# Performance work log

Measured on AMD Instinct MI355X. Metric: run time of the kernel, lower is better.

Reference implementation:

```python
import jax, jax.numpy as jnp
import numpy as np

B, S, D = 8, 4096, 768
HEADS = 12
NEIGHBORS = 2
DILATION = 1
KERNEL = 1 + 2 * NEIGHBORS  # 5
DIM_HEAD = D // HEADS


def setup_inputs() -> dict:
    key = jax.random.key(0)
    ks = jax.random.split(key, 11)
    sc = 1.0 / np.sqrt(D)
    return {
        "x": jax.random.normal(ks[0], (B, S, D), dtype=jnp.float32),
        "Wq": jax.random.normal(ks[1], (D, D), dtype=jnp.float32) * sc,
        "bq": jax.random.normal(ks[2], (D,), dtype=jnp.float32) * 0.02,
        "Wk": jax.random.normal(ks[3], (D, D), dtype=jnp.float32) * sc,
        "bk": jax.random.normal(ks[4], (D,), dtype=jnp.float32) * 0.02,
        "Wv": jax.random.normal(ks[5], (D, D), dtype=jnp.float32) * sc,
        "bv": jax.random.normal(ks[6], (D,), dtype=jnp.float32) * 0.02,
        "Wo": jax.random.normal(ks[7], (D, D), dtype=jnp.float32) * sc,
        "bo": jax.random.normal(ks[8], (D,), dtype=jnp.float32) * 0.02,
        "gamma": jnp.ones((D,), dtype=jnp.float32),
        "beta": jnp.zeros((D,), dtype=jnp.float32),
    }


def _extract_seq_patches(x, kernel_size, dilation):
    # [B, S, D] -> [B, S, kernel_size, D] of dilated local windows, zero-padded.
    seq_len = x.shape[1]
    patch_size = kernel_size + (dilation - 1) * (kernel_size - 1)
    pad_r = (patch_size - 1) // 2
    pad_l = patch_size - pad_r - 1
    xp = jnp.pad(x, ((0, 0), (pad_l, pad_r), (0, 0)))
    # small fixed loop over kernel positions (kernel_size = 5)
    return jnp.stack([xp[:, i:i + seq_len] for i in range(0, patch_size, dilation)], axis=2)


def reference(x, Wq, bq, Wk, bk, Wv, bv, Wo, bo, gamma, beta):
    patches = _extract_seq_patches(x, KERNEL, DILATION)  # [B, S, K, D]
    q = x @ Wq + bq                                       # [B, S, D]
    k = patches @ Wk + bk                                 # [B, S, K, D]
    v = patches @ Wv + bv                                 # [B, S, K, D]
    # split heads
    q = q.reshape(B, S, HEADS, DIM_HEAD)
    k = k.reshape(B, S, KERNEL, HEADS, DIM_HEAD)
    v = v.reshape(B, S, KERNEL, HEADS, DIM_HEAD)
    scale = jnp.sqrt(jnp.asarray(DIM_HEAD, dtype=q.dtype))
    scores = jnp.einsum('bshd,bskhd->bshk', q, k) / scale  # [B, S, H, K]
    p = jax.nn.softmax(scores, axis=-1)
    att = jnp.einsum('bshk,bskhd->bshd', p, v)             # [B, S, H, dh]
    att = att.reshape(B, S, D)
    att = att @ Wo + bo
    y = att + x
    # LayerNorm over last dim
    mu = jnp.mean(y, axis=-1, keepdims=True)
    var = jnp.var(y, axis=-1, keepdims=True)
    y = (y - mu) / jnp.sqrt(var + 1e-5) * gamma + beta
    return y
```

## Files before the change

kernel.cpp:

```cpp
#include <hip/hip_runtime.h>

#define B_  8
#define S_  4096
#define D_  768
#define H_  12
#define M_  (B_ * S_)
#define NQKV_ 2304
#define NTILES 12

typedef unsigned short u16;
typedef __attribute__((ext_vector_type(4))) float  f32x4;
typedef __attribute__((ext_vector_type(8))) __bf16 bf16x8;
typedef __attribute__((ext_vector_type(4))) u16    u16x4;

#define GAS __attribute__((address_space(1)))
#define LAS __attribute__((address_space(3)))

__device__ __forceinline__ u16 f2bf(float f) {
    unsigned u = __float_as_uint(f);
    u += 0x7FFF + ((u >> 16) & 1);
    return (u16)(u >> 16);
}
__device__ __forceinline__ float bf2f(u16 h) {
    return __uint_as_float(((unsigned)h) << 16);
}

__device__ __forceinline__ void gload_lds16(const void* g, void* l) {
    __builtin_amdgcn_global_load_lds((const GAS void*)g, (LAS void*)l, 16, 0, 0);
}

__device__ __forceinline__ int xcd_swz(int bid, int nwg) {
    return (bid & 7) * (nwg >> 3) + (bid >> 3);
}

__global__ __launch_bounds__(256) void castx_kernel(const float* __restrict__ x,
                                                    u16* __restrict__ xb) {
    const int i = blockIdx.x * 256 + threadIdx.x;
    const float4 v = ((const float4*)x)[i];
    u16x4 o;
    o.x = f2bf(v.x); o.y = f2bf(v.y); o.z = f2bf(v.z); o.w = f2bf(v.w);
    ((u16x4*)xb)[i] = o;
}

__global__ __launch_bounds__(256) void wtrans_kernel(const float* __restrict__ Wq,
                                                     const float* __restrict__ Wk,
                                                     const float* __restrict__ Wv,
                                                     const float* __restrict__ Wo,
                                                     u16* __restrict__ Wb) {
    const float* W = (blockIdx.z == 0) ? Wq : (blockIdx.z == 1) ? Wk
                   : (blockIdx.z == 2) ? Wv : Wo;
    u16* O = Wb + (size_t)blockIdx.z * D_ * D_;
    __shared__ float tile[32][33];
    const int tx = threadIdx.x & 31, ty = threadIdx.x >> 5;
    const int k0 = blockIdx.y * 32, n0 = blockIdx.x * 32;
#pragma unroll
    for (int j = 0; j < 4; j++)
        tile[ty + j * 8][tx] = W[(size_t)(k0 + ty + j * 8) * D_ + n0 + tx];
    __syncthreads();
#pragma unroll
    for (int j = 0; j < 4; j++)
        O[(size_t)(n0 + ty + j * 8) * D_ + k0 + tx] = f2bf(tile[tx][ty + j * 8]);
}


#define MFMA8(AF, BF)                                                        \
    __builtin_amdgcn_s_setprio(1);                                           \
    _Pragma("unroll") for (int mi = 0; mi < 4; ++mi)                         \
        _Pragma("unroll") for (int ni = 0; ni < 2; ++ni)                     \
            acc[mi][ni] = __builtin_amdgcn_mfma_f32_16x16x32_bf16(           \
                AF[mi], BF[ni], acc[mi][ni], 0, 0, 0);                       \
    __builtin_amdgcn_s_setprio(0)

#define RD(p, imm) (*(const bf16x8*)((p) + (imm)))

template <int MODE>
__global__ __launch_bounds__(512, 4) void gemm2_kernel(
    const u16* __restrict__ A, const u16* __restrict__ Wb,
    const float* __restrict__ b0, const float* __restrict__ b1,
    const float* __restrict__ b2,
    u16* __restrict__ outb, const u16* __restrict__ xres) {
    extern __shared__ char lds[];

    const int t = threadIdx.x;
    const int w = t >> 6, l = t & 63;
    const int wm = w >> 2, wn = w & 3;

    const int NTN = (MODE == 0) ? 18 : 6;
    const int work = xcd_swz(blockIdx.x, gridDim.x);
    const int mt = work / NTN, nt = work % NTN;
    const int m0 = mt * 128;
    const int col0 = nt * 128;
    const int widx = (MODE == 0) ? (nt / 6) : 3;
    const int n0w  = (MODE == 0) ? (nt % 6) * 128 : col0;

    const int sr = w * 16 + (l >> 3);
    const int sc = l & 7;
    const int schunk = sc ^ (sr & 7);
    const u16* Asrc = A + (size_t)(m0 + sr) * D_ + schunk * 8;
    const u16* Bsrc = Wb + (size_t)widx * (D_ * D_)
                         + (size_t)(n0w + sr) * D_ + schunk * 8;
    char* const dstA = lds + w * 2048;
    char* const dstB = lds + 16384 + w * 2048;

    const int ck0 = (((l >> 4) ^ (l & 7)) << 4);
    const int ck1 = ((((l >> 4) + 4) ^ (l & 7)) << 4);
    const char* aB = lds + (wm * 64 + (l & 15)) * 128;
    const char* bB = lds + 16384 + (wn * 32 + (l & 15)) * 128;

    f32x4 acc[4][2];
#pragma unroll
    for (int i = 0; i < 4; i++)
#pragma unroll
        for (int j = 0; j < 2; j++) acc[i][j] = (f32x4){0.f, 0.f, 0.f, 0.f};

    auto STAGE = [&](int tk, int b) {
        const int ko = tk * 64;
        char* da = dstA + b * 32768;
        char* db = dstB + b * 32768;
        gload_lds16(Asrc + ko, da);
        gload_lds16(Asrc + ko + 8 * D_, da + 1024);
        gload_lds16(Bsrc + ko, db);
        gload_lds16(Bsrc + ko + 8 * D_, db + 1024);
    };

    STAGE(0, 0);
    __syncthreads();

#pragma unroll
    for (int X = 0; X < NTILES; ++X) {
        const int cb = (X & 1) * 32768;
        if (X + 1 < NTILES) STAGE(X + 1, (X & 1) ^ 1);

        bf16x8 af[4], bf[2];
#pragma unroll
        for (int mi = 0; mi < 4; ++mi) af[mi] = RD(aB, cb + mi * 2048 + ck0);
#pragma unroll
        for (int ni = 0; ni < 2; ++ni) bf[ni] = RD(bB, cb + ni * 2048 + ck0);
        MFMA8(af, bf);
#pragma unroll
        for (int mi = 0; mi < 4; ++mi) af[mi] = RD(aB, cb + mi * 2048 + ck1);
#pragma unroll
        for (int ni = 0; ni < 2; ++ni) bf[ni] = RD(bB, cb + ni * 2048 + ck1);
        MFMA8(af, bf);

        __syncthreads();
    }

    const int crow0 = m0 + wm * 64 + ((l >> 4) << 2);
    const int ccol0 = col0 + wn * 32 + (l & 15);
    if (MODE == 0) {
        const float* bias = (widx == 0) ? b0 : (widx == 1) ? b1 : b2;
        const int bcol0 = ccol0 - widx * D_;
#pragma unroll
        for (int mi = 0; mi < 4; ++mi)
#pragma unroll
            for (int ni = 0; ni < 2; ++ni) {
                const float bv = bias[bcol0 + ni * 16];
#pragma unroll
                for (int r = 0; r < 4; ++r)
                    outb[(size_t)(crow0 + mi * 16 + r) * NQKV_ + ccol0 + ni * 16] =
                        f2bf(acc[mi][ni][r] + bv);
            }
    } else {
#pragma unroll
        for (int mi = 0; mi < 4; ++mi)
#pragma unroll
            for (int ni = 0; ni < 2; ++ni) {
                const int col = ccol0 + ni * 16;
                const float bv = b0[col];
#pragma unroll
                for (int r = 0; r < 4; ++r) {
                    const size_t idx = (size_t)(crow0 + mi * 16 + r) * D_ + col;
                    outb[idx] = f2bf(acc[mi][ni][r] + bv + bf2f(xres[idx]));
                }
            }
    }
}

__global__ __launch_bounds__(256) void attn_kernel(const u16* __restrict__ QKV,
                                                   const float* __restrict__ bk,
                                                   const float* __restrict__ bv,
                                                   u16* __restrict__ att) {
    const int gw = xcd_swz(blockIdx.x, gridDim.x) * 4 + (threadIdx.x >> 6);
    const int l  = threadIdx.x & 63;
    const int hq = gw % 3;
    const int m  = gw / 3;
    const int s  = m & (S_ - 1);
    const int col = hq * 256 + l * 4;
    const u16* base = QKV + (size_t)m * NQKV_;

    const u16x4 qv = *(const u16x4*)(base + col);
    float qf[4];
#pragma unroll
    for (int j = 0; j < 4; j++) qf[j] = bf2f(qv[j]);

    float sc[5];
#pragma unroll
    for (int i = 0; i < 5; i++) {
        const int sp = s + i - 2;
        float p;
        if (sp >= 0 && sp < S_) {
            const u16x4 kv = *(const u16x4*)(base + (i - 2) * NQKV_ + D_ + col);
            p = qf[0] * bf2f(kv[0]) + qf[1] * bf2f(kv[1])
              + qf[2] * bf2f(kv[2]) + qf[3] * bf2f(kv[3]);
        } else {
            const float4 kb = *(const float4*)(bk + col);
            p = qf[0] * kb.x + qf[1] * kb.y + qf[2] * kb.z + qf[3] * kb.w;
        }
#pragma unroll
        for (int off = 1; off < 16; off <<= 1) p += __shfl_xor(p, off, 64);
        sc[i] = p * 0.125f;
    }
    float mx = sc[0];
#pragma unroll
    for (int i = 1; i < 5; i++) mx = fmaxf(mx, sc[i]);
    float e[5], sum = 0.f;
#pragma unroll
    for (int i = 0; i < 5; i++) { e[i] = __expf(sc[i] - mx); sum += e[i]; }
    const float inv = 1.f / sum;

    float o[4] = {0.f, 0.f, 0.f, 0.f};
#pragma unroll
    for (int i = 0; i < 5; i++) {
        const float wgt = e[i] * inv;
        const int sp = s + i - 2;
        if (sp >= 0 && sp < S_) {
            const u16x4 vv = *(const u16x4*)(base + (i - 2) * NQKV_ + 2 * D_ + col);
#pragma unroll
            for (int j = 0; j < 4; j++) o[j] += wgt * bf2f(vv[j]);
        } else {
            const float4 vb = *(const float4*)(bv + col);
            o[0] += wgt * vb.x; o[1] += wgt * vb.y;
            o[2] += wgt * vb.z; o[3] += wgt * vb.w;
        }
    }
    u16x4 ov;
#pragma unroll
    for (int j = 0; j < 4; j++) ov[j] = f2bf(o[j]);
    *(u16x4*)(att + (size_t)m * D_ + col) = ov;
}

__global__ __launch_bounds__(256) void ln_kernel(const u16* __restrict__ Yb,
                                                 const float* __restrict__ gamma,
                                                 const float* __restrict__ beta,
                                                 float* __restrict__ out) {
    const int row = blockIdx.x;
    const u16* r = Yb + (size_t)row * D_;
    const int t = threadIdx.x;
    const float v0 = bf2f(r[t]), v1 = bf2f(r[t + 256]), v2 = bf2f(r[t + 512]);
    float s  = v0 + v1 + v2;
    float s2 = v0 * v0 + v1 * v1 + v2 * v2;
#pragma unroll
    for (int off = 32; off > 0; off >>= 1) {
        s  += __shfl_xor(s,  off, 64);
        s2 += __shfl_xor(s2, off, 64);
    }
    __shared__ float red[8];
    const int w = t >> 6, l = t & 63;
    if (l == 0) { red[w] = s; red[4 + w] = s2; }
    __syncthreads();
    s  = red[0] + red[1] + red[2] + red[3];
    s2 = red[4] + red[5] + red[6] + red[7];
    const float mu  = s * (1.f / 768.f);
    const float var = s2 * (1.f / 768.f) - mu * mu;
    const float inv = rsqrtf(var + 1e-5f);
    float* o = out + (size_t)row * D_;
    o[t]       = (v0 - mu) * inv * gamma[t]       + beta[t];
    o[t + 256] = (v1 - mu) * inv * gamma[t + 256] + beta[t + 256];
    o[t + 512] = (v2 - mu) * inv * gamma[t + 512] + beta[t + 512];
}

extern "C" void kernel_launch(void* const* d_in, const int* in_sizes, int n_in,
                              void* d_out, int out_size, void* d_ws, size_t ws_size,
                              hipStream_t stream) {
    const float* x     = (const float*)d_in[0];
    const float* Wq    = (const float*)d_in[1];
    const float* bq    = (const float*)d_in[2];
    const float* Wk    = (const float*)d_in[3];
    const float* bk    = (const float*)d_in[4];
    const float* Wv    = (const float*)d_in[5];
    const float* bv    = (const float*)d_in[6];
    const float* Wo    = (const float*)d_in[7];
    const float* bo    = (const float*)d_in[8];
    const float* gamma = (const float*)d_in[9];
    const float* beta  = (const float*)d_in[10];

    char* ws = (char*)d_ws;
    u16*   Wb  = (u16*)ws;
    u16*   xb  = (u16*)(ws + 4718592);
    u16*   QKV = (u16*)(ws + 4718592 + 50331648);
    u16*   yb  = QKV;
    u16*   att = (u16*)d_out;

    (void)hipFuncSetAttribute(reinterpret_cast<const void*>(&gemm2_kernel<0>),
                              hipFuncAttributeMaxDynamicSharedMemorySize, 65536);
    (void)hipFuncSetAttribute(reinterpret_cast<const void*>(&gemm2_kernel<1>),
                              hipFuncAttributeMaxDynamicSharedMemorySize, 65536);

    castx_kernel<<<(M_ * D_) / (256 * 4), 256, 0, stream>>>(x, xb);
    wtrans_kernel<<<dim3(24, 24, 4), 256, 0, stream>>>(Wq, Wk, Wv, Wo, Wb);
    gemm2_kernel<0><<<(M_ / 128) * 18, 512, 65536, stream>>>(xb, Wb, bq, bk, bv,
                                                             QKV, nullptr);
    attn_kernel<<<(M_ * 3) / 4, 256, 0, stream>>>(QKV, bk, bv, att);
    gemm2_kernel<1><<<(M_ / 128) * 6, 512, 65536, stream>>>(att, Wb, bo, nullptr, nullptr,
                                                            yb, xb);
    ln_kernel<<<M_, 256, 0, stream>>>(yb, gamma, beta, (float*)d_out);
}
```

Baseline: 294.4 us.

## Make GEMM kernels persistent with cross-tile prefetch of next tile's first K-slice

Both projection GEMMs now launch 512 persistent blocks, each handling a contiguous run of output tiles (9 for QKV, 3 for output projection). The first K-slice of the next tile is staged into LDS while the last slice of the current tile is computed, and the epilogue runs inside the final K iteration. The aim is to hide per-tile prologue latency and reduce block launch overhead. In exchange, occupancy drops to one wave of blocks, tail balance is fixed, and the xcd swizzle now maps to contiguous work ranges, which may change L2 reuse.

```diff
diff --git a/kernel.cpp b/kernel.cpp
--- a/kernel.cpp
+++ b/kernel.cpp
@@ -74,7 +74,7 @@
 #define RD(p, imm) (*(const bf16x8*)((p) + (imm)))
 
 template <int MODE>
-__global__ __launch_bounds__(512, 4) void gemm2_kernel(
+__global__ __launch_bounds__(512, 4) void gemmp_kernel(
     const u16* __restrict__ A, const u16* __restrict__ Wb,
     const float* __restrict__ b0, const float* __restrict__ b1,
     const float* __restrict__ b2,
@@ -86,94 +86,115 @@
     const int wm = w >> 2, wn = w & 3;
 
     const int NTN = (MODE == 0) ? 18 : 6;
-    const int work = xcd_swz(blockIdx.x, gridDim.x);
-    const int mt = work / NTN, nt = work % NTN;
-    const int m0 = mt * 128;
-    const int col0 = nt * 128;
-    const int widx = (MODE == 0) ? (nt / 6) : 3;
-    const int n0w  = (MODE == 0) ? (nt % 6) * 128 : col0;
-
-    const int sr = w * 16 + (l >> 3);
-    const int sc = l & 7;
-    const int schunk = sc ^ (sr & 7);
-    const u16* Asrc = A + (size_t)(m0 + sr) * D_ + schunk * 8;
-    const u16* Bsrc = Wb + (size_t)widx * (D_ * D_)
-                         + (size_t)(n0w + sr) * D_ + schunk * 8;
-    char* const dstA = lds + w * 2048;
-    char* const dstB = lds + 16384 + w * 2048;
+    const int NW  = (MODE == 0) ? 9 : 3;
+    int work = xcd_swz(blockIdx.x, gridDim.x) * NW;
+
+    const int lrow = l >> 3;
+    const int schunk = (l & 7) ^ lrow;
 
     const int ck0 = (((l >> 4) ^ (l & 7)) << 4);
     const int ck1 = ((((l >> 4) + 4) ^ (l & 7)) << 4);
     const char* aB = lds + (wm * 64 + (l & 15)) * 128;
     const char* bB = lds + 16384 + (wn * 32 + (l & 15)) * 128;
 
+    int m0, col0, widx;
+    const u16 *As, *Bs;
+    auto setp = [&](int wk, int& _m0, int& _col0, int& _widx,
+                    const u16*& _As, const u16*& _Bs) {
+        const int mt = wk / NTN, nt = wk % NTN;
+        _m0 = mt * 128;
+        _col0 = nt * 128;
+        _widx = (MODE == 0) ? (nt / 6) : 3;
+        const int n0w = (MODE == 0) ? (nt % 6) * 128 : _col0;
+        _As = A + (size_t)(_m0 + w * 16 + lrow) * D_ + schunk * 8;
+        _Bs = Wb + (size_t)_widx * (D_ * D_)
+                 + (size_t)(n0w + w * 16 + lrow) * D_ + schunk * 8;
+    };
+    setp(work, m0, col0, widx, As, Bs);
+
+    auto STAGE = [&](const u16* _A, const u16* _B, int kt, int bo) {
+        const int ko = kt * 64;
+        char* da = lds + bo + w * 2048;
+        char* db = lds + bo + 16384 + w * 2048;
+        gload_lds16(_A + ko, da);
+        gload_lds16(_A + ko + 8 * D_, da + 1024);
+        gload_lds16(_B + ko, db);
+        gload_lds16(_B + ko + 8 * D_, db + 1024);
+    };
+
     f32x4 acc[4][2];
 #pragma unroll
     for (int i = 0; i < 4; i++)
 #pragma unroll
         for (int j = 0; j < 2; j++) acc[i][j] = (f32x4){0.f, 0.f, 0.f, 0.f};
 
-    auto STAGE = [&](int tk, int b) {
-        const int ko = tk * 64;
-        char* da = dstA + b * 32768;
-        char* db = dstB + b * 32768;
-        gload_lds16(Asrc + ko, da);
-        gload_lds16(Asrc + ko + 8 * D_, da + 1024);
-        gload_lds16(Bsrc + ko, db);
-        gload_lds16(Bsrc + ko + 8 * D_, db + 1024);
-    };
-
-    STAGE(0, 0);
+    STAGE(As, Bs, 0, 0);
     __syncthreads();
 
-#pragma unroll
-    for (int X = 0; X < NTILES; ++X) {
-        const int cb = (X & 1) * 32768;
-        if (X + 1 < NTILES) STAGE(X + 1, (X & 1) ^ 1);
-
-        bf16x8 af[4], bf[2];
-#pragma unroll
-        for (int mi = 0; mi < 4; ++mi) af[mi] = RD(aB, cb + mi * 2048 + ck0);
-#pragma unroll
-        for (int ni = 0; ni < 2; ++ni) bf[ni] = RD(bB, cb + ni * 2048 + ck0);
-        MFMA8(af, bf);
-#pragma unroll
-        for (int mi = 0; mi < 4; ++mi) af[mi] = RD(aB, cb + mi * 2048 + ck1);
-#pragma unroll
-        for (int ni = 0; ni < 2; ++ni) bf[ni] = RD(bB, cb + ni * 2048 + ck1);
-        MFMA8(af, bf);
-
-        __syncthreads();
-    }
-
-    const int crow0 = m0 + wm * 64 + ((l >> 4) << 2);
-    const int ccol0 = col0 + wn * 32 + (l & 15);
-    if (MODE == 0) {
-        const float* bias = (widx == 0) ? b0 : (widx == 1) ? b1 : b2;
-        const int bcol0 = ccol0 - widx * D_;
-#pragma unroll
-        for (int mi = 0; mi < 4; ++mi)
-#pragma unroll
-            for (int ni = 0; ni < 2; ++ni) {
-                const float bv = bias[bcol0 + ni * 16];
-#pragma unroll
-                for (int r = 0; r < 4; ++r)
-                    outb[(size_t)(crow0 + mi * 16 + r) * NQKV_ + ccol0 + ni * 16] =
-                        f2bf(acc[mi][ni][r] + bv);
+    for (int j = 0; j < NW; ++j) {
+        int nm0 = m0, ncol0 = col0, nwidx = widx;
+        const u16 *nAs = As, *nBs = Bs;
+        if (j + 1 < NW) setp(work + 1, nm0, ncol0, nwidx, nAs, nBs);
+
+#pragma unroll
+        for (int kt = 0; kt < 12; ++kt) {
+            const int cb = (kt & 1) * 32768;
+            const int ob = cb ^ 32768;
+            if (kt < 11)          STAGE(As, Bs, kt + 1, ob);
+            else if (j + 1 < NW)  STAGE(nAs, nBs, 0, ob);
+
+            bf16x8 af[4], bf[2];
+#pragma unroll
+            for (int mi = 0; mi < 4; ++mi) af[mi] = RD(aB, cb + mi * 2048 + ck0);
+#pragma unroll
+            for (int ni = 0; ni < 2; ++ni) bf[ni] = RD(bB, cb + ni * 2048 + ck0);
+            MFMA8(af, bf);
+#pragma unroll
+            for (int mi = 0; mi < 4; ++mi) af[mi] = RD(aB, cb + mi * 2048 + ck1);
+#pragma unroll
+            for (int ni = 0; ni < 2; ++ni) bf[ni] = RD(bB, cb + ni * 2048 + ck1);
+            MFMA8(af, bf);
+
+            if (kt == 11) {
+                const int crow0 = m0 + wm * 64 + ((l >> 4) << 2);
+                const int ccol0 = col0 + wn * 32 + (l & 15);
+                if (MODE == 0) {
+                    const float* bias = (widx == 0) ? b0 : (widx == 1) ? b1 : b2;
+                    const int bcol0 = ccol0 - widx * D_;
+#pragma unroll
+                    for (int mi = 0; mi < 4; ++mi)
+#pragma unroll
+                        for (int ni = 0; ni < 2; ++ni) {
+                            const float bv = bias[bcol0 + ni * 16];
+#pragma unroll
+                            for (int r = 0; r < 4; ++r)
+                                outb[(size_t)(crow0 + mi * 16 + r) * NQKV_
+                                     + ccol0 + ni * 16] = f2bf(acc[mi][ni][r] + bv);
+                        }
+                } else {
+#pragma unroll
+                    for (int mi = 0; mi < 4; ++mi)
+#pragma unroll
+                        for (int ni = 0; ni < 2; ++ni) {
+                            const int col = ccol0 + ni * 16;
+                            const float bv = b0[col];
+#pragma unroll
+                            for (int r = 0; r < 4; ++r) {
+                                const size_t idx =
+                                    (size_t)(crow0 + mi * 16 + r) * D_ + col;
+                                outb[idx] = f2bf(acc[mi][ni][r] + bv + bf2f(xres[idx]));
+                            }
+                        }
+                }
+#pragma unroll
+                for (int i = 0; i < 4; i++)
+#pragma unroll
+                    for (int jj = 0; jj < 2; jj++)
+                        acc[i][jj] = (f32x4){0.f, 0.f, 0.f, 0.f};
             }
-    } else {
-#pragma unroll
-        for (int mi = 0; mi < 4; ++mi)
-#pragma unroll
-            for (int ni = 0; ni < 2; ++ni) {
-                const int col = ccol0 + ni * 16;
-                const float bv = b0[col];
-#pragma unroll
-                for (int r = 0; r < 4; ++r) {
-                    const size_t idx = (size_t)(crow0 + mi * 16 + r) * D_ + col;
-                    outb[idx] = f2bf(acc[mi][ni][r] + bv + bf2f(xres[idx]));
-                }
-            }
+            __syncthreads();
+        }
+        m0 = nm0; col0 = ncol0; widx = nwidx; As = nAs; Bs = nBs; ++work;
     }
 }
 
@@ -292,17 +313,16 @@
     u16*   yb  = QKV;
     u16*   att = (u16*)d_out;
 
-    (void)hipFuncSetAttribute(reinterpret_cast<const void*>(&gemm2_kernel<0>),
+    (void)hipFuncSetAttribute(reinterpret_cast<const void*>(&gemmp_kernel<0>),
                               hipFuncAttributeMaxDynamicSharedMemorySize, 65536);
-    (void)hipFuncSetAttribute(reinterpret_cast<const void*>(&gemm2_kernel<1>),
+    (void)hipFuncSetAttribute(reinterpret_cast<const void*>(&gemmp_kernel<1>),
                               hipFuncAttributeMaxDynamicSharedMemorySize, 65536);
 
     castx_kernel<<<(M_ * D_) / (256 * 4), 256, 0, stream>>>(x, xb);
     wtrans_kernel<<<dim3(24, 24, 4), 256, 0, stream>>>(Wq, Wk, Wv, Wo, Wb);
-    gemm2_kernel<0><<<(M_ / 128) * 18, 512, 65536, stream>>>(xb, Wb, bq, bk, bv,
-                                                             QKV, nullptr);
+    gemmp_kernel<0><<<512, 512, 65536, stream>>>(xb, Wb, bq, bk, bv, QKV, nullptr);
     attn_kernel<<<(M_ * 3) / 4, 256, 0, stream>>>(QKV, bk, bv, att);
-    gemm2_kernel<1><<<(M_ / 128) * 6, 512, 65536, stream>>>(att, Wb, bo, nullptr, nullptr,
-                                                            yb, xb);
+    gemmp_kernel<1><<<512, 512, 65536, stream>>>(att, Wb, bo, nullptr, nullptr,
+                                                 yb, xb);
     ln_kernel<<<M_, 256, 0, stream>>>(yb, gamma, beta, (float*)d_out);
 }
```

Result: slower. 320.1 us (+8.7%).
